# Kernel tuning notes

Measured on AMD Instinct MI355X. Metric: run time of the kernel, lower is better.

The kernel has to match this reference:

```python
import jax, jax.numpy as jnp
import numpy as np

MASK_PENALTY = 1e15  # matches the TF module's additive mask constant


def setup_inputs() -> dict:
    key = jax.random.key(0)
    k1, k2, k3, k4, k5 = jax.random.split(key, 5)
    B, S, E, DK, DV = 4, 2048, 1024, 128, 128
    inputs = jax.random.normal(k1, (B, S, E), dtype=jnp.float32)
    mask = jax.random.randint(k2, (B, S, S), 0, 2, dtype=jnp.int32)
    # Dense kernels (glorot-ish scale)
    Wq = jax.random.normal(k3, (E, DK), dtype=jnp.float32) / np.float32(np.sqrt(E))
    Wk = jax.random.normal(k4, (E, DK), dtype=jnp.float32) / np.float32(np.sqrt(E))
    Wv = jax.random.normal(k5, (E, DV), dtype=jnp.float32) / np.float32(np.sqrt(E))
    return {"inputs": inputs, "mask": mask, "Wq": Wq, "Wk": Wk, "Wv": Wv}


def reference(inputs, mask, Wq, Wk, Wv):
    # q, k, v projections (no bias)
    q = jnp.einsum("bse,ed->bsd", inputs, Wq)  # [B,S,DK]
    k = jnp.einsum("bse,ed->bsd", inputs, Wk)  # [B,S,DK]
    v = jnp.einsum("bse,ed->bsd", inputs, Wv)  # [B,S,DV]
    dim_k = Wq.shape[-1]
    scale = jnp.asarray(1.0 / np.sqrt(dim_k), dtype=q.dtype)
    dot_p = jnp.einsum("bqd,bkd->bqk", q, k) * scale  # [B,S,S]
    dot_p = dot_p - MASK_PENALTY * mask.astype(dot_p.dtype)
    softm = jax.nn.softmax(dot_p, axis=-1)
    return jnp.einsum("bqk,bkd->bqd", softm, v)  # [B,S,DV]
```

## Files before the change

### kernel.cpp

```cpp
#include <hip/hip_runtime.h>
#include <stdint.h>


#define SEQ   2048
#define EDIM  1024
#define DDIM  128
#define QSCALE 0.08838834764831845f

typedef unsigned short u16;
typedef unsigned int   u32;
using short8 = __attribute__((ext_vector_type(8))) short;
using f32x4  = __attribute__((ext_vector_type(4))) float;
using int4v  = __attribute__((ext_vector_type(4))) int;

__device__ __forceinline__ u16 f2bf(float x) {
    uint32_t u = __float_as_uint(x);
    return (u16)((u + 0x7fffu + ((u >> 16) & 1u)) >> 16);
}

__device__ __forceinline__ void gld16(const void* gsrc, void* lds_dst) {
    __builtin_amdgcn_global_load_lds(
        (const __attribute__((address_space(1))) uint32_t*)(uintptr_t)gsrc,
        (__attribute__((address_space(3))) uint32_t*)(uint32_t)(uintptr_t)lds_dst,
        16, 0, 0);
}

__global__ __launch_bounds__(256) void prep_kernel(
    const int* __restrict__ mask,
    const float* __restrict__ Wq, const float* __restrict__ Wk, const float* __restrict__ Wv,
    u32* __restrict__ Mbits, u16* __restrict__ Wt)
{
    __shared__ u32 nib32[2048];
    __shared__ u16 tl[64][65];
    const int bx = blockIdx.x;
    const int tid = threadIdx.x;
    if (bx < 2048) {
        const int* src = mask + (size_t)bx * 8192;
#pragma unroll
        for (int it = 0; it < 8; ++it) {
            const int idx = it * 256 + tid;
            const int4v v = *(const int4v*)(src + idx * 4);
            const u32 nb = (v[0] != 0 ? 1u : 0u) | (v[1] != 0 ? 2u : 0u)
                         | (v[2] != 0 ? 4u : 0u) | (v[3] != 0 ? 8u : 0u);
            nib32[(idx & 7) * 256 + ((idx >> 3) ^ ((idx & 7) << 2))] = nb;
        }
        __syncthreads();
        u32 word = 0;
#pragma unroll
        for (int j = 0; j < 8; ++j)
            word |= (nib32[j * 256 + (tid ^ (j << 2))] & 0xFu) << (4 * j);
        Mbits[bx * 256 + tid] = word;
    } else {
        const int t = bx - 2048;
        const int wsel = t >> 5;
        const int tile = t & 31;
        const int k0 = (tile >> 1) * 64;
        const int n0 = (tile & 1) * 64;
        const float* W = (wsel == 0) ? Wq : ((wsel == 1) ? Wk : Wv);
#pragma unroll
        for (int it = 0; it < 16; ++it) {
            const int idx = it * 256 + tid;
            const int r = idx >> 6, c = idx & 63;
            tl[c][r] = f2bf(W[(size_t)(k0 + r) * DDIM + n0 + c]);
        }
        __syncthreads();
        u16* Wtp = Wt + (size_t)wsel * DDIM * EDIM;
#pragma unroll
        for (int it = 0; it < 16; ++it) {
            const int idx = it * 256 + tid;
            const int r = idx >> 6, c = idx & 63;
            Wtp[(size_t)(n0 + r) * EDIM + k0 + c] = tl[r][c];
        }
    }
}

__global__ __launch_bounds__(256, 3) void proj_kernel(
    const float* __restrict__ Ain, const u16* __restrict__ Wtb,
    u16* __restrict__ Qb, u16* __restrict__ Kb, u16* __restrict__ Vtb)
{
    __shared__ __align__(16) uint8_t smem[20480];
    const int tid = threadIdx.x;
    const int w = tid >> 6, lane = tid & 63;
    const int lq = lane & 15, lg = lane >> 4;

    const int bid = blockIdx.x;
    const int wg = (bid & 7) * 96 + (bid >> 3);
    const int wm = wg % 3;
    const int m0 = (wg / 3) * 32;
    const u16* Wt = Wtb + (size_t)wm * DDIM * EDIM;

    f32x4 acc[2][2] = {};

#pragma unroll 1
    for (int kt = 0; kt < 16; ++kt) {
        const int k0 = kt * 64;
#pragma unroll
        for (int i = 0; i < 4; ++i) {
            const int G = i * 256 + tid;
            const int n = G >> 3, c = G & 7;
            gld16(Wt + (size_t)n * EDIM + k0 + ((c ^ (n & 7)) << 3),
                  smem + 4096 + i * 4096 + w * 1024);
        }
        {
            const int row = tid >> 3, c = tid & 7;
            const float* s2 = Ain + (size_t)(m0 + row) * EDIM + k0 + ((c ^ (row & 7)) << 3);
            const f32x4 a0 = *(const f32x4*)s2;
            const f32x4 a1 = *(const f32x4*)(s2 + 4);
            short8 v;
            v[0] = (short)f2bf(a0[0]); v[1] = (short)f2bf(a0[1]);
            v[2] = (short)f2bf(a0[2]); v[3] = (short)f2bf(a0[3]);
            v[4] = (short)f2bf(a1[0]); v[5] = (short)f2bf(a1[1]);
            v[6] = (short)f2bf(a1[2]); v[7] = (short)f2bf(a1[3]);
            *(short8*)(smem + row * 128 + (c << 4)) = v;
        }
        __syncthreads();
#pragma unroll
        for (int ks = 0; ks < 2; ++ks) {
            short8 af[2], bfv[2];
#pragma unroll
            for (int mf = 0; mf < 2; ++mf) {
                const int arow = mf * 16 + lq;
                af[mf] = *(const short8*)(smem + arow * 128 + ((((ks << 2) + lg) ^ (arow & 7)) << 4));
            }
#pragma unroll
            for (int nf = 0; nf < 2; ++nf) {
                const int brow = w * 32 + nf * 16 + lq;
                bfv[nf] = *(const short8*)(smem + 4096 + brow * 128 + ((((ks << 2) + lg) ^ (brow & 7)) << 4));
            }
#pragma unroll
            for (int mf = 0; mf < 2; ++mf)
#pragma unroll
                for (int nf = 0; nf < 2; ++nf)
                    acc[mf][nf] = __builtin_amdgcn_mfma_f32_16x16x32_bf16(af[mf], bfv[nf], acc[mf][nf], 0, 0, 0);
        }
        __syncthreads();
    }

    const float osc = (wm == 0) ? QSCALE : 1.0f;
    if (wm < 2) {
#pragma unroll
        for (int mf = 0; mf < 2; ++mf)
#pragma unroll
            for (int nf = 0; nf < 2; ++nf)
#pragma unroll
                for (int rr = 0; rr < 4; ++rr) {
                    const int row = mf * 16 + lg * 4 + rr;
                    const int col = w * 32 + nf * 16 + lq;
                    *(u16*)(smem + row * 256 + (((col >> 3) ^ (row & 7)) << 4) + ((col & 7) << 1))
                        = f2bf(acc[mf][nf][rr] * osc);
                }
        __syncthreads();
        u16* dst = (wm == 0 ? Qb : Kb) + (size_t)m0 * 128;
#pragma unroll
        for (int i = 0; i < 2; ++i) {
            const int j = i * 256 + tid;
            const int row = j >> 4, c = j & 15;
            *(short8*)(dst + (size_t)row * 128 + c * 8)
                = *(const short8*)(smem + row * 256 + ((c ^ (row & 7)) << 4));
        }
    } else {
#pragma unroll
        for (int mf = 0; mf < 2; ++mf)
#pragma unroll
            for (int nf = 0; nf < 2; ++nf)
#pragma unroll
                for (int rr = 0; rr < 4; ++rr) {
                    const int sl = mf * 16 + lg * 4 + rr;
                    const int d  = w * 32 + nf * 16 + lq;
                    *(u16*)(smem + d * 64 + (((sl >> 3) ^ (d & 3)) << 4) + ((sl & 7) << 1))
                        = f2bf(acc[mf][nf][rr]);
                }
        __syncthreads();
        const int b = m0 >> 11, s0b = m0 & 2047;
        u16* dst = Vtb + (size_t)b * DDIM * SEQ;
#pragma unroll
        for (int i = 0; i < 2; ++i) {
            const int j = i * 256 + tid;
            const int dd = j >> 2, c = j & 3;
            *(short8*)(dst + (size_t)dd * SEQ + s0b + c * 8)
                = *(const short8*)(smem + dd * 64 + ((c ^ (dd & 3)) << 4));
        }
    }
}

__global__ __launch_bounds__(256, 2) void flash_kernel(
    const u32* __restrict__ Mb,
    const u16* __restrict__ Qb, const u16* __restrict__ Kb, const u16* __restrict__ Vtb,
    float* __restrict__ out)
{
    __shared__ __align__(16) uint8_t smem[36864];
    __shared__ float ml_m[4][16], ml_l[4][16], recipL[16];

    const int tid = threadIdx.x;
    const int w = tid >> 6, lane = tid & 63;
    const int lq = lane & 15, lg = lane >> 4;

    const int bid = blockIdx.x;
    const int qt = (bid & 7) * 64 + (bid >> 3);
    const int b = qt >> 7;
    const int q0 = (qt & 127) << 4;
    const size_t qrow0 = (size_t)b * SEQ + q0;

    const u16* Qp = Qb + qrow0 * 128;
    const u16* Kp = Kb + (size_t)b * SEQ * 128;
    const u16* Vp = Vtb + (size_t)b * DDIM * SEQ;
    const u32* mrp = Mb + (qrow0 + lq) * 64 + w * 16;

    short8 qf[4];
#pragma unroll
    for (int ks = 0; ks < 4; ++ks)
        qf[ks] = *(const short8*)(Qp + (size_t)lq * 128 + ks * 32 + lg * 8);

    f32x4 acc[8] = {};
    float m = -1e30f, l = 0.0f;

    const int kv00 = w * 512;
    short8 kf[2][4], vf[8];
    u32 mw;
#pragma unroll
    for (int nf = 0; nf < 2; ++nf)
#pragma unroll
        for (int ks = 0; ks < 4; ++ks)
            kf[nf][ks] = *(const short8*)(Kp + (size_t)(kv00 + nf * 16 + lq) * 128 + ks * 32 + lg * 8);
#pragma unroll
    for (int df = 0; df < 8; ++df)
        vf[df] = *(const short8*)(Vp + (size_t)(df * 16 + lq) * SEQ + kv00 + lg * 8);
    mw = mrp[0];

    uint8_t* pbase = smem + 32768 + w * 1024;

#pragma unroll 1
    for (int t = 0; t < 16; ++t) {
        const int tn = (t < 15) ? t + 1 : 15;
        const int kvn = kv00 + tn * 32;
        __builtin_amdgcn_sched_barrier(0);
        f32x4 sacc[2] = {};
#pragma unroll
        for (int ks = 0; ks < 4; ++ks)
#pragma unroll
            for (int nf = 0; nf < 2; ++nf)
                sacc[nf] = __builtin_amdgcn_mfma_f32_16x16x32_bf16(kf[nf][ks], qf[ks], sacc[nf], 0, 0, 0);
        __builtin_amdgcn_sched_barrier(0);
#pragma unroll
        for (int nf = 0; nf < 2; ++nf)
#pragma unroll
            for (int ks = 0; ks < 4; ++ks)
                kf[nf][ks] = *(const short8*)(Kp + (size_t)(kvn + nf * 16 + lq) * 128 + ks * 32 + lg * 8);
        __builtin_amdgcn_sched_barrier(0);
        float sv[2][4];
#pragma unroll
        for (int nf = 0; nf < 2; ++nf)
#pragma unroll
            for (int r = 0; r < 4; ++r)
                sv[nf][r] = sacc[nf][r] + (((mw >> (nf * 16 + lg * 4 + r)) & 1u) ? -1e15f : 0.0f);
        float tm = sv[0][0];
#pragma unroll
        for (int nf = 0; nf < 2; ++nf)
#pragma unroll
            for (int r = 0; r < 4; ++r) tm = fmaxf(tm, sv[nf][r]);
        tm = fmaxf(tm, __shfl_xor(tm, 16));
        tm = fmaxf(tm, __shfl_xor(tm, 32));
        const float mnew = fmaxf(m, tm);
        const float sf = __expf(m - mnew);
        m = mnew;
        float p[2][4];
        float rs = 0.0f;
#pragma unroll
        for (int nf = 0; nf < 2; ++nf)
#pragma unroll
            for (int r = 0; r < 4; ++r) { p[nf][r] = __expf(sv[nf][r] - m); rs += p[nf][r]; }
        rs += __shfl_xor(rs, 16);
        rs += __shfl_xor(rs, 32);
        l = l * sf + rs;
        mw = mrp[tn];
#pragma unroll
        for (int df = 0; df < 8; ++df) acc[df] *= sf;
#pragma unroll
        for (int nf = 0; nf < 2; ++nf)
#pragma unroll
            for (int h = 0; h < 2; ++h) {
                const u32 pk = (u32)f2bf(p[nf][2 * h]) | ((u32)f2bf(p[nf][2 * h + 1]) << 16);
                const int kv = lg * 4 + 2 * h + 16 * nf;
                *(u32*)(pbase + lq * 64 + (((kv >> 3) ^ (lq & 3)) << 4) + ((kv << 1) & 15)) = pk;
            }
        const short8 pf = *(const short8*)(pbase + lq * 64 + ((lg ^ (lq & 3)) << 4));
        __builtin_amdgcn_sched_barrier(0);
#pragma unroll
        for (int df = 0; df < 8; ++df)
            acc[df] = __builtin_amdgcn_mfma_f32_16x16x32_bf16(vf[df], pf, acc[df], 0, 0, 0);
        __builtin_amdgcn_sched_barrier(0);
#pragma unroll
        for (int df = 0; df < 8; ++df)
            vf[df] = *(const short8*)(Vp + (size_t)(df * 16 + lq) * SEQ + kvn + lg * 8);
    }

    if (lg == 0) { ml_m[w][lq] = m; ml_l[w][lq] = l; }
    __syncthreads();
    {
        const float m0v = ml_m[0][lq], m1v = ml_m[1][lq], m2v = ml_m[2][lq], m3v = ml_m[3][lq];
        const float mm = fmaxf(fmaxf(m0v, m1v), fmaxf(m2v, m3v));
        const float Lg = ml_l[0][lq] * __expf(m0v - mm) + ml_l[1][lq] * __expf(m1v - mm)
                       + ml_l[2][lq] * __expf(m2v - mm) + ml_l[3][lq] * __expf(m3v - mm);
        const float s = __expf(m - mm);
        if (w == 0 && lg == 0) recipL[lq] = 1.0f / Lg;
        float* Ol = (float*)smem;
#pragma unroll
        for (int df = 0; df < 8; ++df) {
            const f32x4 vsc = acc[df] * s;
            *(f32x4*)(Ol + (size_t)(w * 16 + lq) * 128 + df * 16 + lg * 4) = vsc;
        }
    }
    __syncthreads();
    {
        const float* Ol = (const float*)smem;
        const int row = tid >> 4, c0 = (tid & 15) * 8;
        const float rl = recipL[row];
        f32x4 s0 = {}, s1 = {};
#pragma unroll
        for (int wv = 0; wv < 4; ++wv) {
            const float* p2 = Ol + (size_t)(wv * 16 + row) * 128 + c0;
            s0 += *(const f32x4*)p2;
            s1 += *(const f32x4*)(p2 + 4);
        }
        s0 *= rl; s1 *= rl;
        float* op = out + (qrow0 + row) * 128 + c0;
        *(f32x4*)op = s0;
        *(f32x4*)(op + 4) = s1;
    }
}

extern "C" void kernel_launch(void* const* d_in, const int* in_sizes, int n_in,
                              void* d_out, int out_size, void* d_ws, size_t ws_size,
                              hipStream_t stream) {
    (void)in_sizes; (void)n_in; (void)out_size; (void)ws_size;
    const float* inputs = (const float*)d_in[0];
    const int*   mask   = (const int*)d_in[1];
    const float* Wq     = (const float*)d_in[2];
    const float* Wk     = (const float*)d_in[3];
    const float* Wv     = (const float*)d_in[4];
    float* out = (float*)d_out;

    uint8_t* ws = (uint8_t*)d_ws;
    u16* Wtb   = (u16*)ws;
    u16* Qb    = (u16*)(ws + 786432);
    u16* Kb    = (u16*)(ws + 2883584);
    u16* Vtb   = (u16*)(ws + 4980736);
    u32* Mbits = (u32*)(ws + 7077888);

    hipLaunchKernelGGL(prep_kernel, dim3(2144), dim3(256), 0, stream, mask, Wq, Wk, Wv, Mbits, Wtb);
    hipLaunchKernelGGL(proj_kernel, dim3(768), dim3(256), 0, stream, inputs, Wtb, Qb, Kb, Vtb);
    hipLaunchKernelGGL(flash_kernel, dim3(512), dim3(256), 0, stream, Mbits, Qb, Kb, Vtb, out);
}
```

Baseline: 202.9 us.

## Share K/V tiles across two query groups via LDS double-buffered async loads

The flash kernel now uses 512-thread blocks that handle 32 query rows in two groups of four waves. K and V tiles are staged once into double-buffered LDS with global_load_lds and shared by both query groups, replacing per-wave direct global loads into registers. It also adds lazy rescaling, which skips the max update unless the new max exceeds the old one by more than 8, plus packed bf16 conversion and s_setprio around the MFMAs. In exchange it needs about 136KB of LDS per block, allows only one block per CU, runs half as many blocks, and adds a block barrier on every iteration.

```diff
diff --git a/kernel.cpp b/kernel.cpp
--- a/kernel.cpp
+++ b/kernel.cpp
@@ -183,28 +183,29 @@
     }
 }
 
-__global__ __launch_bounds__(256, 2) void flash_kernel(
+__global__ __launch_bounds__(512, 1) void flash_kernel(
     const u32* __restrict__ Mb,
     const u16* __restrict__ Qb, const u16* __restrict__ Kb, const u16* __restrict__ Vtb,
     float* __restrict__ out)
 {
-    __shared__ __align__(16) uint8_t smem[36864];
-    __shared__ float ml_m[4][16], ml_l[4][16], recipL[16];
+    __shared__ __align__(16) uint8_t smem[139264];
+    __shared__ float ml_m[2][4][16], ml_l[2][4][16], recipL[32];
 
     const int tid = threadIdx.x;
     const int w = tid >> 6, lane = tid & 63;
+    const int qi = w >> 2, ki = w & 3;
     const int lq = lane & 15, lg = lane >> 4;
 
     const int bid = blockIdx.x;
-    const int qt = (bid & 7) * 64 + (bid >> 3);
-    const int b = qt >> 7;
-    const int q0 = (qt & 127) << 4;
+    const int qt = (bid & 7) * 32 + (bid >> 3);
+    const int b = qt >> 6;
+    const int q0 = (qt & 63) << 5;
     const size_t qrow0 = (size_t)b * SEQ + q0;
 
-    const u16* Qp = Qb + qrow0 * 128;
+    const u16* Qp = Qb + (qrow0 + qi * 16) * 128;
     const u16* Kp = Kb + (size_t)b * SEQ * 128;
     const u16* Vp = Vtb + (size_t)b * DDIM * SEQ;
-    const u32* mrp = Mb + (qrow0 + lq) * 64 + w * 16;
+    const u32* mrp = Mb + (qrow0 + qi * 16 + lq) * 64 + ki * 16;
 
     short8 qf[4];
 #pragma unroll
@@ -214,39 +215,53 @@
     f32x4 acc[8] = {};
     float m = -1e30f, l = 0.0f;
 
-    const int kv00 = w * 512;
-    short8 kf[2][4], vf[8];
-    u32 mw;
-#pragma unroll
-    for (int nf = 0; nf < 2; ++nf)
-#pragma unroll
-        for (int ks = 0; ks < 4; ++ks)
-            kf[nf][ks] = *(const short8*)(Kp + (size_t)(kv00 + nf * 16 + lq) * 128 + ks * 32 + lg * 8);
-#pragma unroll
-    for (int df = 0; df < 8; ++df)
-        vf[df] = *(const short8*)(Vp + (size_t)(df * 16 + lq) * SEQ + kv00 + lg * 8);
-    mw = mrp[0];
-
-    uint8_t* pbase = smem + 32768 + w * 1024;
+    uint8_t* kvb0 = smem + ki * 32768;
+    uint8_t* pbase = smem + 131072 + w * 1024;
+
+    auto stage = [&](uint8_t* kvb, int kv0) {
+        if (qi == 0) {
+#pragma unroll
+            for (int i = 0; i < 8; ++i) {
+                const int G = i * 64 + lane;
+                const int row = G >> 4, c = G & 15;
+                gld16(Kp + (size_t)(kv0 + row) * 128 + ((c ^ (row & 7)) << 3),
+                      kvb + i * 1024);
+            }
+        } else {
+#pragma unroll
+            for (int i = 0; i < 8; ++i) {
+                const int G = i * 64 + lane;
+                const int dd = G >> 2, c = G & 3;
+                gld16(Vp + (size_t)dd * SEQ + kv0 + ((c ^ ((dd ^ (dd >> 2)) & 3)) << 3),
+                      kvb + 8192 + i * 1024);
+            }
+        }
+    };
+
+    stage(kvb0, ki * 512);
+    u32 mw = mrp[0];
+    asm volatile("s_waitcnt vmcnt(0)" ::: "memory");
+    __builtin_amdgcn_s_barrier();
 
 #pragma unroll 1
     for (int t = 0; t < 16; ++t) {
-        const int tn = (t < 15) ? t + 1 : 15;
-        const int kvn = kv00 + tn * 32;
+        uint8_t* kvb = kvb0 + (t & 1) * 16384;
+        if (t < 15) stage(kvb0 + ((t + 1) & 1) * 16384, ki * 512 + (t + 1) * 32);
+        const u32 mwn = mrp[(t < 15) ? t + 1 : 15];
         __builtin_amdgcn_sched_barrier(0);
+
         f32x4 sacc[2] = {};
+        __builtin_amdgcn_s_setprio(1);
 #pragma unroll
         for (int ks = 0; ks < 4; ++ks)
 #pragma unroll
-            for (int nf = 0; nf < 2; ++nf)
-                sacc[nf] = __builtin_amdgcn_mfma_f32_16x16x32_bf16(kf[nf][ks], qf[ks], sacc[nf], 0, 0, 0);
-        __builtin_amdgcn_sched_barrier(0);
-#pragma unroll
-        for (int nf = 0; nf < 2; ++nf)
-#pragma unroll
-            for (int ks = 0; ks < 4; ++ks)
-                kf[nf][ks] = *(const short8*)(Kp + (size_t)(kvn + nf * 16 + lq) * 128 + ks * 32 + lg * 8);
-        __builtin_amdgcn_sched_barrier(0);
+            for (int nf = 0; nf < 2; ++nf) {
+                const int krow = nf * 16 + lq;
+                const short8 kf = *(const short8*)(kvb + krow * 256 + ((((ks << 2) + lg) ^ (krow & 7)) << 4));
+                sacc[nf] = __builtin_amdgcn_mfma_f32_16x16x32_bf16(kf, qf[ks], sacc[nf], 0, 0, 0);
+            }
+        __builtin_amdgcn_s_setprio(0);
+
         float sv[2][4];
 #pragma unroll
         for (int nf = 0; nf < 2; ++nf)
@@ -260,9 +275,14 @@
             for (int r = 0; r < 4; ++r) tm = fmaxf(tm, sv[nf][r]);
         tm = fmaxf(tm, __shfl_xor(tm, 16));
         tm = fmaxf(tm, __shfl_xor(tm, 32));
-        const float mnew = fmaxf(m, tm);
-        const float sf = __expf(m - mnew);
-        m = mnew;
+        if (!__all(tm <= m + 8.0f)) {
+            const float mnew = fmaxf(m, tm);
+            const float sf = __expf(m - mnew);
+            m = mnew;
+            l *= sf;
+#pragma unroll
+            for (int df = 0; df < 8; ++df) acc[df] *= sf;
+        }
         float p[2][4];
         float rs = 0.0f;
 #pragma unroll
@@ -271,54 +291,61 @@
             for (int r = 0; r < 4; ++r) { p[nf][r] = __expf(sv[nf][r] - m); rs += p[nf][r]; }
         rs += __shfl_xor(rs, 16);
         rs += __shfl_xor(rs, 32);
-        l = l * sf + rs;
-        mw = mrp[tn];
-#pragma unroll
-        for (int df = 0; df < 8; ++df) acc[df] *= sf;
+        l += rs;
+        mw = mwn;
+
 #pragma unroll
         for (int nf = 0; nf < 2; ++nf)
 #pragma unroll
             for (int h = 0; h < 2; ++h) {
-                const u32 pk = (u32)f2bf(p[nf][2 * h]) | ((u32)f2bf(p[nf][2 * h + 1]) << 16);
-                const int kv = lg * 4 + 2 * h + 16 * nf;
+                u32 pk;
+                asm("v_cvt_pk_bf16_f32 %0, %1, %2" : "=v"(pk) : "v"(p[nf][2 * h]), "v"(p[nf][2 * h + 1]));
+                const int kv = nf * 16 + lg * 4 + 2 * h;
                 *(u32*)(pbase + lq * 64 + (((kv >> 3) ^ (lq & 3)) << 4) + ((kv << 1) & 15)) = pk;
             }
         const short8 pf = *(const short8*)(pbase + lq * 64 + ((lg ^ (lq & 3)) << 4));
-        __builtin_amdgcn_sched_barrier(0);
-#pragma unroll
-        for (int df = 0; df < 8; ++df)
-            acc[df] = __builtin_amdgcn_mfma_f32_16x16x32_bf16(vf[df], pf, acc[df], 0, 0, 0);
-        __builtin_amdgcn_sched_barrier(0);
-#pragma unroll
-        for (int df = 0; df < 8; ++df)
-            vf[df] = *(const short8*)(Vp + (size_t)(df * 16 + lq) * SEQ + kvn + lg * 8);
-    }
-
-    if (lg == 0) { ml_m[w][lq] = m; ml_l[w][lq] = l; }
+
+        __builtin_amdgcn_s_setprio(1);
+#pragma unroll
+        for (int df = 0; df < 8; ++df) {
+            const int dd = df * 16 + lq;
+            const short8 vf = *(const short8*)(kvb + 8192 + dd * 64 + ((lg ^ ((dd ^ (dd >> 2)) & 3)) << 4));
+            acc[df] = __builtin_amdgcn_mfma_f32_16x16x32_bf16(vf, pf, acc[df], 0, 0, 0);
+        }
+        __builtin_amdgcn_s_setprio(0);
+
+        asm volatile("s_waitcnt vmcnt(0)" ::: "memory");
+        __builtin_amdgcn_s_barrier();
+    }
+
+    if (lg == 0) { ml_m[qi][ki][lq] = m; ml_l[qi][ki][lq] = l; }
     __syncthreads();
     {
-        const float m0v = ml_m[0][lq], m1v = ml_m[1][lq], m2v = ml_m[2][lq], m3v = ml_m[3][lq];
+        const float m0v = ml_m[qi][0][lq], m1v = ml_m[qi][1][lq];
+        const float m2v = ml_m[qi][2][lq], m3v = ml_m[qi][3][lq];
         const float mm = fmaxf(fmaxf(m0v, m1v), fmaxf(m2v, m3v));
-        const float Lg = ml_l[0][lq] * __expf(m0v - mm) + ml_l[1][lq] * __expf(m1v - mm)
-                       + ml_l[2][lq] * __expf(m2v - mm) + ml_l[3][lq] * __expf(m3v - mm);
+        const float Lg = ml_l[qi][0][lq] * __expf(m0v - mm) + ml_l[qi][1][lq] * __expf(m1v - mm)
+                       + ml_l[qi][2][lq] * __expf(m2v - mm) + ml_l[qi][3][lq] * __expf(m3v - mm);
+        if (ki == 0 && lg == 0) recipL[qi * 16 + lq] = 1.0f / Lg;
         const float s = __expf(m - mm);
-        if (w == 0 && lg == 0) recipL[lq] = 1.0f / Lg;
         float* Ol = (float*)smem;
+        float* dstq = Ol + ((size_t)(qi * 4 + ki) * 16 + lq) * 132;
 #pragma unroll
         for (int df = 0; df < 8; ++df) {
             const f32x4 vsc = acc[df] * s;
-            *(f32x4*)(Ol + (size_t)(w * 16 + lq) * 128 + df * 16 + lg * 4) = vsc;
+            *(f32x4*)(dstq + df * 16 + lg * 4) = vsc;
         }
     }
     __syncthreads();
     {
         const float* Ol = (const float*)smem;
         const int row = tid >> 4, c0 = (tid & 15) * 8;
+        const int rqi = row >> 4, rq = row & 15;
         const float rl = recipL[row];
         f32x4 s0 = {}, s1 = {};
 #pragma unroll
-        for (int wv = 0; wv < 4; ++wv) {
-            const float* p2 = Ol + (size_t)(wv * 16 + row) * 128 + c0;
+        for (int kk = 0; kk < 4; ++kk) {
+            const float* p2 = Ol + ((size_t)(rqi * 4 + kk) * 16 + rq) * 132 + c0;
             s0 += *(const f32x4*)p2;
             s1 += *(const f32x4*)(p2 + 4);
         }
@@ -349,5 +376,5 @@
 
     hipLaunchKernelGGL(prep_kernel, dim3(2144), dim3(256), 0, stream, mask, Wq, Wk, Wv, Mbits, Wtb);
     hipLaunchKernelGGL(proj_kernel, dim3(768), dim3(256), 0, stream, inputs, Wtb, Qb, Kb, Vtb);
-    hipLaunchKernelGGL(flash_kernel, dim3(512), dim3(256), 0, stream, Mbits, Qb, Kb, Vtb, out);
-}
+    hipLaunchKernelGGL(flash_kernel, dim3(256), dim3(512), 0, stream, Mbits, Qb, Kb, Vtb, out);
+}
```

New measurement: 170.3 us. 1.19x faster.
